# Optimization experiments

Measured on AMD Instinct MI355X. Metric: run time of the kernel, lower is better.

The kernel has to match this reference:

```python
import jax, jax.numpy as jnp
import numpy as np

ALPHA = 0.1  # init kwarg alpha


def setup_inputs() -> dict:
    key = jax.random.key(0)
    k1, k2 = jax.random.split(key)
    x = jax.random.normal(k1, (32, 192, 64, 64), dtype=jnp.float32)
    delta = jax.random.normal(k2, (32, 1, 64, 64), dtype=jnp.float32)
    return {"x_bchw": x, "delta": delta}


def reference(x_bchw, delta):
    # Faithful fixed-shape version of LayerTokenPrune.forward.
    # Kept tokens are stream-compacted to the front (stable, preserving
    # original token order, matching torch.where index order); dropped
    # positions are zero-padded, matching the zero-pad in the original.
    B, C, H, W = x_bchw.shape
    L = H * W
    tok = jnp.transpose(x_bchw, (0, 2, 3, 1)).reshape(B, L, C)  # [B, L, C]

    delta_tok = delta.reshape(B, -1)  # 4-dim delta branch -> [B, L]
    imp = jnp.abs(delta_tok)
    lo = imp.min(axis=1, keepdims=True)
    hi = imp.max(axis=1, keepdims=True)
    rng = jnp.maximum(hi - lo, 1e-3)  # clamp_min(0.001)
    imp = (imp - lo) / rng

    mu = imp.mean(axis=1, keepdims=True)
    sigma = imp.std(axis=1, keepdims=True, ddof=1)  # torch std is unbiased
    theta = mu - ALPHA * sigma
    keep = imp >= theta  # [B, L] bool; max-imp token always kept (theta<=mu<=1)

    # Stable compaction: kept token indices first, in original order.
    # jnp.argsort is stable, so sorting the key (0 for keep, 1 for drop)
    # reproduces torch.where's ascending-index order for kept tokens.
    order = jnp.argsort(jnp.logical_not(keep).astype(jnp.int32), axis=1)  # [B, L]
    gathered = jnp.take_along_axis(tok, order[:, :, None], axis=1)  # [B, L, C]

    counts = keep.sum(axis=1)  # [B]
    valid = (jnp.arange(L)[None, :] < counts[:, None]).astype(tok.dtype)  # [B, L]
    tok_new = gathered * valid[:, :, None]  # zero out pad positions

    # Fixed-shape analogue of the sqrt reshape: pad to full L = H*W grid.
    y = tok_new.reshape(B, H, W, C).transpose(0, 3, 1, 2)  # [B, C, H, W]

    keep_ratio = counts.astype(jnp.float32).mean() / L
    theta_mean = theta.mean()
    return y, keep_ratio, theta_mean
```

## Files before the change

kernel.cpp:

```cpp
#include <hip/hip_runtime.h>
#include <hip/hip_bf16.h>
#include <math.h>

#define B_ 32
#define C_ 192
#define H_ 64
#define W_ 64
#define L_ 4096
#define L4_ 1024
#define NTHREADS 256
#define PER_THREAD 16
#define CPB 6

#define SWIZ(i) ((((i) & 3) << 10) | ((i) >> 2))

__global__ __launch_bounds__(NTHREADS) void stats_scan_kernel(
    const float* __restrict__ delta,
    int*  __restrict__ src_idx,
    int*  __restrict__ counts,
    float* __restrict__ thetas)
{
  const int b = blockIdx.x;
  const int t = threadIdx.x;
  const int lane = t & 63;
  const int wid  = t >> 6;

  __shared__ float  smin[4], smax[4];
  __shared__ float  s_lo, s_rng, s_theta;
  __shared__ double dsum[4], dsum2[4];
  __shared__ int    wsum[4];

  const float* dp = delta + (size_t)b * L_;

  float a[PER_THREAD];
  const float4* d4 = (const float4*)dp;
  #pragma unroll
  for (int i = 0; i < 4; ++i) {
    float4 v = d4[t * 4 + i];
    a[i*4+0] = fabsf(v.x); a[i*4+1] = fabsf(v.y);
    a[i*4+2] = fabsf(v.z); a[i*4+3] = fabsf(v.w);
  }

  float lmin = a[0], lmax = a[0];
  #pragma unroll
  for (int i = 1; i < PER_THREAD; ++i) {
    lmin = fminf(lmin, a[i]);
    lmax = fmaxf(lmax, a[i]);
  }
  #pragma unroll
  for (int off = 32; off; off >>= 1) {
    lmin = fminf(lmin, __shfl_down(lmin, off, 64));
    lmax = fmaxf(lmax, __shfl_down(lmax, off, 64));
  }
  if (lane == 0) { smin[wid] = lmin; smax[wid] = lmax; }
  __syncthreads();
  if (t == 0) {
    float lo = fminf(fminf(smin[0], smin[1]), fminf(smin[2], smin[3]));
    float hi = fmaxf(fmaxf(smax[0], smax[1]), fmaxf(smax[2], smax[3]));
    s_lo  = lo;
    s_rng = fmaxf(hi - lo, 1e-3f);
  }
  __syncthreads();
  const float lo  = s_lo;
  const float rng = s_rng;

  double s = 0.0, s2 = 0.0;
  #pragma unroll
  for (int i = 0; i < PER_THREAD; ++i) {
    float imp = (a[i] - lo) / rng;
    a[i] = imp;
    s  += (double)imp;
    s2 += (double)imp * (double)imp;
  }
  #pragma unroll
  for (int off = 32; off; off >>= 1) {
    s  += __shfl_down(s,  off, 64);
    s2 += __shfl_down(s2, off, 64);
  }
  if (lane == 0) { dsum[wid] = s; dsum2[wid] = s2; }
  __syncthreads();
  if (t == 0) {
    double S  = dsum[0]  + dsum[1]  + dsum[2]  + dsum[3];
    double S2 = dsum2[0] + dsum2[1] + dsum2[2] + dsum2[3];
    double mu  = S / (double)L_;
    double var = (S2 - S * S / (double)L_) / (double)(L_ - 1);
    if (var < 0.0) var = 0.0;
    double sigma = sqrt(var);
    s_theta = (float)(mu - 0.1 * sigma);
  }
  __syncthreads();
  const float theta = s_theta;

  int flags = 0, cnt = 0;
  #pragma unroll
  for (int i = 0; i < PER_THREAD; ++i) {
    int k = (a[i] >= theta) ? 1 : 0;
    cnt += k;
    flags |= (k << i);
  }
  int inc = cnt;
  #pragma unroll
  for (int off = 1; off < 64; off <<= 1) {
    int y = __shfl_up(inc, off, 64);
    if (lane >= off) inc += y;
  }
  if (lane == 63) wsum[wid] = inc;
  __syncthreads();
  int base = inc - cnt;
  #pragma unroll
  for (int w = 0; w < 4; ++w)
    if (w < wid) base += wsum[w];

  int* sb = src_idx + (size_t)b * L_;
  int p = base;
  #pragma unroll
  for (int i = 0; i < PER_THREAD; ++i) {
    if ((flags >> i) & 1) { sb[p++] = t * PER_THREAD + i; }
  }
  if (t == NTHREADS - 1) {
    counts[b] = base + cnt;
    thetas[b] = theta;
  }
}

__global__ __launch_bounds__(64) void finalize_kernel(
    const int* __restrict__ counts, const float* __restrict__ thetas,
    float* __restrict__ out_tail)
{
  const int t = threadIdx.x;
  float c  = (t < B_) ? (float)counts[t] : 0.0f;
  float th = (t < B_) ? thetas[t]        : 0.0f;
  #pragma unroll
  for (int off = 32; off; off >>= 1) {
    c  += __shfl_down(c,  off, 64);
    th += __shfl_down(th, off, 64);
  }
  if (t == 0) {
    out_tail[0] = (c / (float)B_) / (float)L_;
    out_tail[1] = th / (float)B_;
  }
}

__global__ __launch_bounds__(NTHREADS) void gather_kernel(
    const float* __restrict__ x,
    const int*  __restrict__ src_idx,
    const int*  __restrict__ counts,
    float* __restrict__ out)
{
  __shared__ float buf[2][L_];

  const int gidx = blockIdx.x;
  const int b  = gidx >> 5;
  const int c0 = (gidx & 31) * CPB;
  const int t  = threadIdx.x;

  const int cnt = counts[b];

  const int4* s4b = (const int4*)(src_idx + (size_t)b * L_);
  int4 s[4];
  #pragma unroll
  for (int i = 0; i < 4; ++i) s[i] = s4b[t + NTHREADS * i];

  const float* xrow0 = x   + ((size_t)b * C_ + c0) * L_;
  float*       orow0 = out + ((size_t)b * C_ + c0) * L_;

  {
    const float4* x4 = (const float4*)xrow0;
    #pragma unroll
    for (int i = 0; i < 4; ++i) {
      const int j = t + NTHREADS * i;
      float4 v = x4[j];
      buf[0][(0 << 10) | j] = v.x;
      buf[0][(1 << 10) | j] = v.y;
      buf[0][(2 << 10) | j] = v.z;
      buf[0][(3 << 10) | j] = v.w;
    }
  }

  #pragma unroll
  for (int k = 0; k < CPB; ++k) {
    __syncthreads();

    float4 v[4];
    if (k + 1 < CPB) {
      const float4* x4 = (const float4*)(xrow0 + (size_t)(k + 1) * L_);
      #pragma unroll
      for (int i = 0; i < 4; ++i) v[i] = x4[t + NTHREADS * i];
    }

    const float* rb = buf[k & 1];
    float4* o4 = (float4*)(orow0 + (size_t)k * L_);
    #pragma unroll
    for (int i = 0; i < 4; ++i) {
      const int j  = t + NTHREADS * i;
      const int d0 = j * 4;
      const int4 si = s[i];
      float4 r;
      r.x = (d0 + 0 < cnt) ? rb[SWIZ(si.x)] : 0.0f;
      r.y = (d0 + 1 < cnt) ? rb[SWIZ(si.y)] : 0.0f;
      r.z = (d0 + 2 < cnt) ? rb[SWIZ(si.z)] : 0.0f;
      r.w = (d0 + 3 < cnt) ? rb[SWIZ(si.w)] : 0.0f;
      o4[j] = r;
    }

    if (k + 1 < CPB) {
      float* wb = buf[(k + 1) & 1];
      #pragma unroll
      for (int i = 0; i < 4; ++i) {
        const int j = t + NTHREADS * i;
        wb[(0 << 10) | j] = v[i].x;
        wb[(1 << 10) | j] = v[i].y;
        wb[(2 << 10) | j] = v[i].z;
        wb[(3 << 10) | j] = v[i].w;
      }
    }
  }
}

extern "C" void kernel_launch(void* const* d_in, const int* in_sizes, int n_in,
                              void* d_out, int out_size, void* d_ws, size_t ws_size,
                              hipStream_t stream) {
  const float* x     = (const float*)d_in[0];
  const float* delta = (const float*)d_in[1];
  float* out = (float*)d_out;

  int*   src_idx = (int*)d_ws;
  int*   counts  = (int*)((char*)d_ws + (size_t)B_ * L_ * 4);
  float* thetas  = (float*)((char*)d_ws + (size_t)B_ * L_ * 4 + 128);

  const size_t y_elems = (size_t)B_ * C_ * L_;

  stats_scan_kernel<<<B_, NTHREADS, 0, stream>>>(delta, src_idx, counts, thetas);
  finalize_kernel<<<1, 64, 0, stream>>>(counts, thetas, out + y_elems);
  gather_kernel<<<B_ * (C_ / CPB), NTHREADS, 0, stream>>>(x, src_idx, counts, out);
}
```

Baseline: 190.1 us.

## Fold finalize into gather kernel, single LDS buffer, halve channels per block

Moves the tiny finalize reduction into block 0 of the gather kernel, removing one kernel launch. The gather kernel's LDS buffer goes from double to single (32KB to 16KB), with the next channel's data prefetched into registers. Channels per block drop from 6 to 3, doubling the grid to 2048 blocks. Together these aim to raise occupancy and cut launch overhead, at the cost of an extra barrier per channel and less reuse of the index loads per block.

New measurement: 213.8 us. +12.5%, slower.

```diff
diff --git a/kernel.cpp b/kernel.cpp
--- a/kernel.cpp
+++ b/kernel.cpp
@@ -10,7 +10,7 @@
 #define L4_ 1024
 #define NTHREADS 256
 #define PER_THREAD 16
-#define CPB 6
+#define CPB 3
 
 #define SWIZ(i) ((((i) & 3) << 10) | ((i) >> 2))
 
@@ -123,36 +123,34 @@
   }
 }
 
-__global__ __launch_bounds__(64) void finalize_kernel(
-    const int* __restrict__ counts, const float* __restrict__ thetas,
-    float* __restrict__ out_tail)
-{
-  const int t = threadIdx.x;
-  float c  = (t < B_) ? (float)counts[t] : 0.0f;
-  float th = (t < B_) ? thetas[t]        : 0.0f;
-  #pragma unroll
-  for (int off = 32; off; off >>= 1) {
-    c  += __shfl_down(c,  off, 64);
-    th += __shfl_down(th, off, 64);
-  }
-  if (t == 0) {
-    out_tail[0] = (c / (float)B_) / (float)L_;
-    out_tail[1] = th / (float)B_;
-  }
-}
-
 __global__ __launch_bounds__(NTHREADS) void gather_kernel(
     const float* __restrict__ x,
     const int*  __restrict__ src_idx,
     const int*  __restrict__ counts,
-    float* __restrict__ out)
+    const float* __restrict__ thetas,
+    float* __restrict__ out,
+    float* __restrict__ out_tail)
 {
-  __shared__ float buf[2][L_];
+  __shared__ float buf[L_];
 
   const int gidx = blockIdx.x;
-  const int b  = gidx >> 5;
-  const int c0 = (gidx & 31) * CPB;
+  const int b  = gidx >> 6;
+  const int c0 = (gidx & 63) * CPB;
   const int t  = threadIdx.x;
+
+  if (gidx == 0 && t < 64) {
+    float c  = (t < B_) ? (float)counts[t] : 0.0f;
+    float th = (t < B_) ? thetas[t]        : 0.0f;
+    #pragma unroll
+    for (int off = 32; off; off >>= 1) {
+      c  += __shfl_down(c,  off, 64);
+      th += __shfl_down(th, off, 64);
+    }
+    if (t == 0) {
+      out_tail[0] = (c / (float)B_) / (float)L_;
+      out_tail[1] = th / (float)B_;
+    }
+  }
 
   const int cnt = counts[b];
 
@@ -164,55 +162,46 @@
   const float* xrow0 = x   + ((size_t)b * C_ + c0) * L_;
   float*       orow0 = out + ((size_t)b * C_ + c0) * L_;
 
+  float4 r[4];
   {
     const float4* x4 = (const float4*)xrow0;
     #pragma unroll
+    for (int i = 0; i < 4; ++i) r[i] = x4[t + NTHREADS * i];
+  }
+
+  #pragma unroll
+  for (int k = 0; k < CPB; ++k) {
+    if (k > 0) __syncthreads();
+
+    #pragma unroll
     for (int i = 0; i < 4; ++i) {
       const int j = t + NTHREADS * i;
-      float4 v = x4[j];
-      buf[0][(0 << 10) | j] = v.x;
-      buf[0][(1 << 10) | j] = v.y;
-      buf[0][(2 << 10) | j] = v.z;
-      buf[0][(3 << 10) | j] = v.w;
-    }
-  }
-
-  #pragma unroll
-  for (int k = 0; k < CPB; ++k) {
+      buf[(0 << 10) | j] = r[i].x;
+      buf[(1 << 10) | j] = r[i].y;
+      buf[(2 << 10) | j] = r[i].z;
+      buf[(3 << 10) | j] = r[i].w;
+    }
+
+    if (k + 1 < CPB) {
+      const float4* xn = (const float4*)(xrow0 + (size_t)(k + 1) * L_);
+      #pragma unroll
+      for (int i = 0; i < 4; ++i) r[i] = xn[t + NTHREADS * i];
+    }
+
     __syncthreads();
 
-    float4 v[4];
-    if (k + 1 < CPB) {
-      const float4* x4 = (const float4*)(xrow0 + (size_t)(k + 1) * L_);
-      #pragma unroll
-      for (int i = 0; i < 4; ++i) v[i] = x4[t + NTHREADS * i];
-    }
-
-    const float* rb = buf[k & 1];
     float4* o4 = (float4*)(orow0 + (size_t)k * L_);
     #pragma unroll
     for (int i = 0; i < 4; ++i) {
       const int j  = t + NTHREADS * i;
       const int d0 = j * 4;
       const int4 si = s[i];
-      float4 r;
-      r.x = (d0 + 0 < cnt) ? rb[SWIZ(si.x)] : 0.0f;
-      r.y = (d0 + 1 < cnt) ? rb[SWIZ(si.y)] : 0.0f;
-      r.z = (d0 + 2 < cnt) ? rb[SWIZ(si.z)] : 0.0f;
-      r.w = (d0 + 3 < cnt) ? rb[SWIZ(si.w)] : 0.0f;
-      o4[j] = r;
-    }
-
-    if (k + 1 < CPB) {
-      float* wb = buf[(k + 1) & 1];
-      #pragma unroll
-      for (int i = 0; i < 4; ++i) {
-        const int j = t + NTHREADS * i;
-        wb[(0 << 10) | j] = v[i].x;
-        wb[(1 << 10) | j] = v[i].y;
-        wb[(2 << 10) | j] = v[i].z;
-        wb[(3 << 10) | j] = v[i].w;
-      }
+      float4 w;
+      w.x = (d0 + 0 < cnt) ? buf[SWIZ(si.x)] : 0.0f;
+      w.y = (d0 + 1 < cnt) ? buf[SWIZ(si.y)] : 0.0f;
+      w.z = (d0 + 2 < cnt) ? buf[SWIZ(si.z)] : 0.0f;
+      w.w = (d0 + 3 < cnt) ? buf[SWIZ(si.w)] : 0.0f;
+      o4[j] = w;
     }
   }
 }
@@ -231,6 +220,6 @@
   const size_t y_elems = (size_t)B_ * C_ * L_;
 
   stats_scan_kernel<<<B_, NTHREADS, 0, stream>>>(delta, src_idx, counts, thetas);
-  finalize_kernel<<<1, 64, 0, stream>>>(counts, thetas, out + y_elems);
-  gather_kernel<<<B_ * (C_ / CPB), NTHREADS, 0, stream>>>(x, src_idx, counts, out);
+  gather_kernel<<<B_ * (C_ / CPB), NTHREADS, 0, stream>>>(
+      x, src_idx, counts, thetas, out, out + y_elems);
 }
```
